# Performance work log

Measured on AMD Instinct MI355X. Metric: run time of the kernel, lower is better.

The kernel has to match this reference:

```python
import jax, jax.numpy as jnp
import numpy as np

L_IMG, L_TXT, B, C, T, D = 12, 12, 64, 1000, 8, 512


def setup_inputs() -> dict:
    key = jax.random.key(0)
    ks = jax.random.split(key, 8)
    s = 0.05  # keep attention logits in a sane range
    return {
        "x": jax.random.normal(ks[0], (L_IMG, B, D), jnp.float32),                 # per-layer projected CLS feats [L,B,D]
        "text_features": jax.random.normal(ks[1], (C, L_TXT, T, D), jnp.float32),  # precomputed per-class text feats
        "self_in_w": jax.random.normal(ks[2], (3 * D, D), jnp.float32) * s,
        "self_in_b": jnp.zeros((3 * D,), jnp.float32),
        "self_out_w": jax.random.normal(ks[3], (D, D), jnp.float32) * s,
        "self_out_b": jnp.zeros((D,), jnp.float32),
        "cross_in_w": jax.random.normal(ks[4], (3 * D, D), jnp.float32) * s,
        "cross_in_b": jnp.zeros((3 * D,), jnp.float32),
        "cross_out_w": jax.random.normal(ks[5], (D, D), jnp.float32) * s,
        "cross_out_b": jnp.zeros((D,), jnp.float32),
        "logit_scale": jnp.full((1,), np.log(1.0 / 0.07), jnp.float32),
    }


def reference(x, text_features, self_in_w, self_in_b, self_out_w, self_out_b,
              cross_in_w, cross_in_b, cross_out_w, cross_out_b, logit_scale):
    d = x.shape[-1]
    scale = 1.0 / jnp.sqrt(jnp.asarray(d, x.dtype))

    # ---- self-attention over the layer axis (torch MHA, 1 head, seq-first [L,B,D]) ----
    Wq, Wk, Wv = jnp.split(self_in_w, 3, axis=0)
    bq, bk, bv = jnp.split(self_in_b, 3, axis=0)
    q = jnp.einsum('lbd,ed->lbe', x, Wq) + bq
    k = jnp.einsum('lbd,ed->lbe', x, Wk) + bk
    v = jnp.einsum('lbd,ed->lbe', x, Wv) + bv
    attn = jax.nn.softmax(jnp.einsum('lbe,mbe->blm', q, k) * scale, axis=-1)
    xs = jnp.einsum('blm,mbe->lbe', attn, v) @ self_out_w.T + self_out_b   # [L,B,D]
    image_features = xs[-1]                                               # [B,D]

    # ---- batched cross-attention: query = image layer-tokens, key/value = per-class,
    #      per-template text layer-tokens; averaged over templates and query layers ----
    cWq, cWk, cWv = jnp.split(cross_in_w, 3, axis=0)
    cbq, cbk, cbv = jnp.split(cross_in_b, 3, axis=0)
    q2 = jnp.einsum('lbd,ed->lbe', xs, cWq) + cbq                          # [L,B,E]
    k2 = jnp.einsum('cmtd,ed->cmte', text_features, cWk) + cbk             # [C,M,T,E]
    v2 = jnp.einsum('cmtd,ed->cmte', text_features, cWv) + cbv
    a2 = jax.nn.softmax(jnp.einsum('lbe,cmte->bctlm', q2, k2) * scale, axis=-1)
    n_avg = a2.shape[2] * a2.shape[3]                                      # T * L_img
    # out_proj is linear, so mean over (template, layer) commutes with it
    ctx = jnp.einsum('bctlm,cmtd->bcd', a2, v2) / n_avg                    # [B,C,D]
    txt = ctx @ cross_out_w.T + cross_out_b                                # [B,C,D]

    # ---- normalize and compute logits (matching the source's permute(1,2,0) + norm(dim=-1)) ----
    tf = jnp.transpose(txt, (0, 2, 1))                                     # [B,D,C]
    img_n = image_features / jnp.linalg.norm(image_features, axis=-1, keepdims=True)
    tf_n = tf / jnp.linalg.norm(tf, axis=-1, keepdims=True)
    return jnp.exp(logit_scale[0]) * jnp.einsum('bd,bdc->bc', img_n, tf_n)  # [B,C]
```

## Files before the change

kernel.cpp:

```cpp
#include <hip/hip_runtime.h>

#define L_IMG 12
#define BATCH 64
#define NCLS  1000
#define DIM   512
#define NTM   96
#define SCALEF 0.044194173824159216f

typedef __attribute__((ext_vector_type(8))) short bf16x8;
typedef __attribute__((ext_vector_type(4))) float f32x4;

__device__ __forceinline__ float bf2f(unsigned short u) {
    return __uint_as_float(((unsigned int)u) << 16);
}
__device__ __forceinline__ unsigned short f2bf(float f) {
    unsigned int u = __float_as_uint(f);
    u += 0x7FFFu + ((u >> 16) & 1u);
    return (unsigned short)(u >> 16);
}
__device__ __forceinline__ void storeo(float* p, float v) { *p = v; }
__device__ __forceinline__ void storeo(unsigned short* p, float v) { *p = f2bf(v); }

__device__ __forceinline__ int swz(int row, int u) {
    return (row << 5) + ((u ^ ((row >> 1) & 3)) << 3);
}

__device__ __forceinline__ void gload16(const unsigned short* g, unsigned short* l) {
    __builtin_amdgcn_global_load_lds(
        (const __attribute__((address_space(1))) void*)g,
        (__attribute__((address_space(3))) void*)l, 16, 0, 0);
}

__global__ __launch_bounds__(256)
void f2bf_kernel(const float* __restrict__ in, unsigned short* __restrict__ out, int n)
{
    int i = (blockIdx.x * 256 + threadIdx.x) * 4;
    if (i < n) {
        float4 v = *(const float4*)(in + i);
        ushort4 o;
        o.x = f2bf(v.x); o.y = f2bf(v.y); o.z = f2bf(v.z); o.w = f2bf(v.w);
        *(ushort4*)(out + i) = o;
    }
}

__global__ __launch_bounds__(256)
void fold_wvo(const float* __restrict__ cow, const float* __restrict__ cWv,
              const float* __restrict__ cbv, const float* __restrict__ cob,
              unsigned short* __restrict__ Wvob, float* __restrict__ bvo)
{
    __shared__ float crow[DIM];
    __shared__ float red[256];
    const int d = blockIdx.x, t = threadIdx.x;
    float c0 = cow[d * DIM + t], c1 = cow[d * DIM + t + 256];
    crow[t] = c0; crow[t + 256] = c1;
    red[t] = c0 * cbv[t] + c1 * cbv[t + 256];
    __syncthreads();
    for (int s = 128; s > 0; s >>= 1) {
        if (t < s) red[t] += red[t + s];
        __syncthreads();
    }
    if (t == 0) bvo[d] = red[0] + cob[d];
    float a0 = 0.f, a1 = 0.f;
    for (int e = 0; e < DIM; e++) {
        float ce = crow[e];
        a0 += ce * cWv[e * DIM + t];
        a1 += ce * cWv[e * DIM + t + 256];
    }
    Wvob[d * DIM + t]       = f2bf(a0);
    Wvob[d * DIM + t + 256] = f2bf(a1);
}

#define BKT 32
#define LDT 68
__global__ __launch_bounds__(256)
void gemm_bt_f32(const float* __restrict__ A, const float* __restrict__ W,
                 const float* __restrict__ bias, float* __restrict__ Co,
                 int M, int N, int K, float out_scale)
{
    __shared__ float As[BKT * LDT];
    __shared__ float Ws[BKT * LDT];
    const int tid = threadIdx.x;
    const int m0 = blockIdx.y << 6, n0 = blockIdx.x << 6;
    const int tx = tid & 15, ty = tid >> 4;
    float acc[4][4] = {};
    for (int k0 = 0; k0 < K; k0 += BKT) {
        #pragma unroll
        for (int i = 0; i < 2; i++) {
            int slot = tid + (i << 8);
            int r = slot >> 3, kq = slot & 7;
            float4 v = *(const float4*)(A + (size_t)(m0 + r) * K + k0 + (kq << 2));
            As[(kq*4+0)*LDT + r] = v.x; As[(kq*4+1)*LDT + r] = v.y;
            As[(kq*4+2)*LDT + r] = v.z; As[(kq*4+3)*LDT + r] = v.w;
            float4 w = *(const float4*)(W + (size_t)(n0 + r) * K + k0 + (kq << 2));
            Ws[(kq*4+0)*LDT + r] = w.x; Ws[(kq*4+1)*LDT + r] = w.y;
            Ws[(kq*4+2)*LDT + r] = w.z; Ws[(kq*4+3)*LDT + r] = w.w;
        }
        __syncthreads();
        #pragma unroll
        for (int kk = 0; kk < BKT; kk++) {
            float4 a = *(const float4*)(As + kk*LDT + ty*4);
            float4 w = *(const float4*)(Ws + kk*LDT + tx*4);
            acc[0][0] += a.x*w.x; acc[0][1] += a.x*w.y; acc[0][2] += a.x*w.z; acc[0][3] += a.x*w.w;
            acc[1][0] += a.y*w.x; acc[1][1] += a.y*w.y; acc[1][2] += a.y*w.z; acc[1][3] += a.y*w.w;
            acc[2][0] += a.z*w.x; acc[2][1] += a.z*w.y; acc[2][2] += a.z*w.z; acc[2][3] += a.z*w.w;
            acc[3][0] += a.w*w.x; acc[3][1] += a.w*w.y; acc[3][2] += a.w*w.z; acc[3][3] += a.w*w.w;
        }
        __syncthreads();
    }
    #pragma unroll
    for (int i = 0; i < 4; i++) {
        int mr = m0 + ty*4 + i;
        #pragma unroll
        for (int j = 0; j < 4; j++) {
            int n = n0 + tx*4 + j;
            float v = acc[i][j];
            if (bias) v += bias[n];
            Co[(size_t)mr * N + n] = v * out_scale;
        }
    }
}

__global__ __launch_bounds__(256)
void gemm_nt_f32(const float* __restrict__ A, const float* __restrict__ W,
                 float* __restrict__ Co, int M, int N, int K)
{
    __shared__ float As[BKT * LDT];
    __shared__ float Ws[BKT * LDT];
    const int tid = threadIdx.x;
    const int m0 = blockIdx.y << 6, n0 = blockIdx.x << 6;
    const int tx = tid & 15, ty = tid >> 4;
    float acc[4][4] = {};
    for (int k0 = 0; k0 < K; k0 += BKT) {
        #pragma unroll
        for (int i = 0; i < 2; i++) {
            int slot = tid + (i << 8);
            int r = slot >> 3, kq = slot & 7;
            float4 v = *(const float4*)(A + (size_t)(m0 + r) * K + k0 + (kq << 2));
            As[(kq*4+0)*LDT + r] = v.x; As[(kq*4+1)*LDT + r] = v.y;
            As[(kq*4+2)*LDT + r] = v.z; As[(kq*4+3)*LDT + r] = v.w;
            int kr = slot >> 4, c4 = slot & 15;
            *(float4*)(Ws + kr*LDT + c4*4) =
                *(const float4*)(W + (size_t)(k0 + kr) * N + n0 + (c4 << 2));
        }
        __syncthreads();
        #pragma unroll
        for (int kk = 0; kk < BKT; kk++) {
            float4 a = *(const float4*)(As + kk*LDT + ty*4);
            float4 w = *(const float4*)(Ws + kk*LDT + tx*4);
            acc[0][0] += a.x*w.x; acc[0][1] += a.x*w.y; acc[0][2] += a.x*w.z; acc[0][3] += a.x*w.w;
            acc[1][0] += a.y*w.x; acc[1][1] += a.y*w.y; acc[1][2] += a.y*w.z; acc[1][3] += a.y*w.w;
            acc[2][0] += a.z*w.x; acc[2][1] += a.z*w.y; acc[2][2] += a.z*w.z; acc[2][3] += a.z*w.w;
            acc[3][0] += a.w*w.x; acc[3][1] += a.w*w.y; acc[3][2] += a.w*w.z; acc[3][3] += a.w*w.w;
        }
        __syncthreads();
    }
    #pragma unroll
    for (int i = 0; i < 4; i++) {
        int mr = m0 + ty*4 + i;
        #pragma unroll
        for (int j = 0; j < 4; j++)
            Co[(size_t)mr * N + n0 + tx*4 + j] = acc[i][j];
    }
}

__global__ __launch_bounds__(256)
void attn_kernel(const float* __restrict__ qkv, float* __restrict__ ao)
{
    __shared__ float lq[L_IMG * DIM];
    __shared__ float lk[L_IMG * DIM];
    __shared__ float sc[L_IMG * L_IMG];
    __shared__ float sa[L_IMG * L_IMG];
    const int b = blockIdx.x, tid = threadIdx.x;
    for (int i = 0; i < 6; i++) {
        int slot = tid + (i << 8);
        int l = slot >> 7, e4 = slot & 127;
        const float* row = qkv + (size_t)(l * BATCH + b) * 1536;
        *(float4*)(lq + l*DIM + e4*4) = *(const float4*)(row + e4*4);
        *(float4*)(lk + l*DIM + e4*4) = *(const float4*)(row + DIM + e4*4);
    }
    __syncthreads();
    if (tid < 144) {
        int l = tid / 12, m = tid % 12;
        float a = 0.f;
        for (int d4 = 0; d4 < 128; d4++) {
            float4 q = *(const float4*)(lq + l*DIM + d4*4);
            float4 k = *(const float4*)(lk + m*DIM + d4*4);
            a += q.x*k.x + q.y*k.y + q.z*k.z + q.w*k.w;
        }
        sc[tid] = a * SCALEF;
    }
    __syncthreads();
    if (tid < 12) {
        float mx = -1e30f;
        for (int m = 0; m < 12; m++) mx = fmaxf(mx, sc[tid*12 + m]);
        float e[12], s = 0.f;
        for (int m = 0; m < 12; m++) { e[m] = __expf(sc[tid*12 + m] - mx); s += e[m]; }
        float inv = 1.f / s;
        for (int m = 0; m < 12; m++) sa[tid*12 + m] = e[m] * inv;
    }
    __syncthreads();
    for (int i = 0; i < 2; i++) {
        int e = tid + (i << 8);
        float vv[12];
        #pragma unroll
        for (int m = 0; m < 12; m++)
            vv[m] = qkv[(size_t)(m * BATCH + b) * 1536 + 1024 + e];
        #pragma unroll
        for (int l = 0; l < 12; l++) {
            float a = 0.f;
            #pragma unroll
            for (int m = 0; m < 12; m++) a += sa[l*12 + m] * vv[m];
            ao[(size_t)(l * BATCH + b) * DIM + e] = a;
        }
    }
}

__global__ __launch_bounds__(256)
void img_kernel(const float* __restrict__ xs, float* __restrict__ imgn)
{
    __shared__ float red[256];
    const int b = blockIdx.x, tid = threadIdx.x;
    const float* row = xs + (size_t)(11 * BATCH + b) * DIM;
    float v0 = row[tid], v1 = row[tid + 256];
    red[tid] = v0*v0 + v1*v1;
    __syncthreads();
    for (int s = 128; s > 0; s >>= 1) {
        if (tid < s) red[tid] += red[tid + s];
        __syncthreads();
    }
    float inv = rsqrtf(red[0]);
    imgn[b*DIM + tid]       = v0 * inv;
    imgn[b*DIM + tid + 256] = v1 * inv;
}

__global__ __launch_bounds__(256)
void build_q2p(const float* __restrict__ q2s, unsigned short* __restrict__ q2pb)
{
    const int l = blockIdx.x, b = blockIdx.y, t = threadIdx.x;
    int d0 = t * 2;
    unsigned int o = 0;
    if (l < 12) {
        float2 v = *(const float2*)(q2s + (size_t)(l * BATCH + b) * DIM + d0);
        o = (unsigned int)f2bf(v.x) | ((unsigned int)f2bf(v.y) << 16);
    }
    ((unsigned int*)q2pb)[(size_t)(b * 16 + l) * 256 + t] = o;
}

template<typename OutT>
__global__ __launch_bounds__(256, 4)
void gemm_mfma(const unsigned short* __restrict__ A, const unsigned short* __restrict__ W,
               const float* __restrict__ bias, OutT* __restrict__ Co,
               int M, int N, float scale)
{
    const int K = DIM;
    __shared__ __align__(16) unsigned short AsBuf[2][128 * 32];
    __shared__ __align__(16) unsigned short WsBuf[2][128 * 32];
    const int m0 = blockIdx.y << 7, n0 = blockIdx.x << 7;
    const int tid = threadIdx.x;
    const int w = tid >> 6, lane = tid & 63;
    const int mt0 = (w & 1) * 4, nt0 = (w >> 1) * 4;
    const int r16 = lane & 15, kq = lane >> 4;
    const int row0 = (w << 5) + (lane >> 2), row1 = row0 + 16;
    const int sc0 = ((lane & 3) ^ ((row0 >> 1) & 3)) << 3;
    const int sc1 = ((lane & 3) ^ ((row1 >> 1) & 3)) << 3;
    const unsigned short* gA0 = A + (size_t)(m0 + row0) * K + sc0;
    const unsigned short* gA1 = A + (size_t)(m0 + row1) * K + sc1;
    const unsigned short* gW0 = W + (size_t)(n0 + row0) * K + sc0;
    const unsigned short* gW1 = W + (size_t)(n0 + row1) * K + sc1;
    const int lw = w << 10;
    int offa[4], offb[4];
    #pragma unroll
    for (int i = 0; i < 4; i++) {
        offa[i] = swz((mt0 + i) * 16 + r16, kq);
        offb[i] = swz((nt0 + i) * 16 + r16, kq);
    }
    f32x4 acc[4][4] = {};

    gload16(gA0, AsBuf[0] + lw);
    gload16(gA1, AsBuf[0] + lw + 512);
    gload16(gW0, WsBuf[0] + lw);
    gload16(gW1, WsBuf[0] + lw + 512);
    __syncthreads();

    #pragma unroll
    for (int t = 0; t < 16; t++) {
        const int cur = t & 1, nxt = cur ^ 1;
        if (t < 15) {
            const int ko = (t + 1) << 5;
            gload16(gA0 + ko, AsBuf[nxt] + lw);
            gload16(gA1 + ko, AsBuf[nxt] + lw + 512);
            gload16(gW0 + ko, WsBuf[nxt] + lw);
            gload16(gW1 + ko, WsBuf[nxt] + lw + 512);
        }
        bf16x8 af[4], bfr[4];
        #pragma unroll
        for (int i = 0; i < 4; i++) {
            af[i]  = *(const bf16x8*)(AsBuf[cur] + offa[i]);
            bfr[i] = *(const bf16x8*)(WsBuf[cur] + offb[i]);
        }
        #pragma unroll
        for (int i = 0; i < 4; i++)
            #pragma unroll
            for (int j = 0; j < 4; j++)
                acc[i][j] = __builtin_amdgcn_mfma_f32_16x16x32_bf16(af[i], bfr[j], acc[i][j], 0, 0, 0);
        if (t < 15) __syncthreads();
    }
    const int rbase = (lane >> 4) * 4;
    #pragma unroll
    for (int i = 0; i < 4; i++)
        #pragma unroll
        for (int j = 0; j < 4; j++) {
            int gcol = n0 + (nt0 + j) * 16 + r16;
            float bv = bias ? bias[gcol] : 0.f;
            #pragma unroll
            for (int r = 0; r < 4; r++) {
                int grow = m0 + (mt0 + i) * 16 + rbase + r;
                storeo(Co + (size_t)grow * N + gcol, acc[i][j][r] * scale + bv);
            }
        }
}

__global__ __launch_bounds__(256, 3)
void fused_scores(const unsigned short* __restrict__ q2pb, const unsigned short* __restrict__ k2,
                  float* __restrict__ wout)
{
    __shared__ __align__(16) unsigned short AsBuf[2][256 * 32];
    __shared__ __align__(16) unsigned short KsBuf[2][96 * 32];
    const int bid = blockIdx.x;
    const int g = bid >> 5, r = bid & 31;
    const int c = g * 8 + (r & 7), bg = r >> 3;
    const int tid = threadIdx.x;
    const int m0 = bg << 8;
    const int w = tid >> 6, lane = tid & 63;
    const int r16 = lane & 15, kq = lane >> 4;
    const size_t kb = (size_t)c * NTM * DIM;
    const int arow = lane >> 2, aun = lane & 3;
    const unsigned short* gAs[4];
    #pragma unroll
    for (int s = 0; s < 4; s++) {
        int rw = (w << 6) + (s << 4) + arow;
        int scx = (aun ^ ((rw >> 1) & 3)) << 3;
        gAs[s] = q2pb + (size_t)(m0 + rw) * DIM + scx;
    }
    const int krow0 = (w << 5) + arow, krow1 = krow0 + 16;
    const int sk0 = (aun ^ ((krow0 >> 1) & 3)) << 3;
    const int sk1 = (aun ^ ((krow1 >> 1) & 3)) << 3;
    const unsigned short* gK0 = k2 + kb + (size_t)krow0 * DIM + sk0;
    const unsigned short* gK1 = k2 + kb + (size_t)krow1 * DIM + sk1;
    const bool kw = (w < 3);
    const int lwA = w << 11;
    const int lwK = w << 10;
    int offa[4], offk[6];
    #pragma unroll
    for (int i = 0; i < 4; i++) offa[i] = swz((w << 6) + i * 16 + r16, kq);
    #pragma unroll
    for (int j = 0; j < 6; j++) offk[j] = swz(j * 16 + r16, kq);
    f32x4 acc[4][6] = {};

    #pragma unroll
    for (int s = 0; s < 4; s++) gload16(gAs[s], AsBuf[0] + lwA + (s << 9));
    if (kw) {
        gload16(gK0, KsBuf[0] + lwK);
        gload16(gK1, KsBuf[0] + lwK + 512);
    }
    __syncthreads();

    #pragma unroll
    for (int t = 0; t < 16; t++) {
        const int cur = t & 1, nxt = cur ^ 1;
        if (t < 15) {
            const int ko = (t + 1) << 5;
            #pragma unroll
            for (int s = 0; s < 4; s++) gload16(gAs[s] + ko, AsBuf[nxt] + lwA + (s << 9));
            if (kw) {
                gload16(gK0 + ko, KsBuf[nxt] + lwK);
                gload16(gK1 + ko, KsBuf[nxt] + lwK + 512);
            }
        }
        bf16x8 af[4], bfr[6];
        #pragma unroll
        for (int i = 0; i < 4; i++)
            af[i] = *(const bf16x8*)(AsBuf[cur] + offa[i]);
        #pragma unroll
        for (int j = 0; j < 6; j++)
            bfr[j] = *(const bf16x8*)(KsBuf[cur] + offk[j]);
        __builtin_amdgcn_s_setprio(1);
        #pragma unroll
        for (int i = 0; i < 4; i++)
            #pragma unroll
            for (int j = 0; j < 6; j++)
                acc[i][j] = __builtin_amdgcn_mfma_f32_16x16x32_bf16(af[i], bfr[j], acc[i][j], 0, 0, 0);
        __builtin_amdgcn_s_setprio(0);
        if (t < 15) __syncthreads();
    }

    #pragma unroll
    for (int i = 0; i < 4; i++) {
        #pragma unroll
        for (int rr = 0; rr < 4; rr++) {
            float v0 = acc[i][0][rr], v1 = acc[i][1][rr], v2 = acc[i][2][rr];
            float v3 = acc[i][3][rr], v4 = acc[i][4][rr], v5 = acc[i][5][rr];
            float mx = fmaxf(fmaxf(fmaxf(v0, v1), fmaxf(v2, v3)), fmaxf(v4, v5));
            mx = fmaxf(mx, __shfl_xor(mx, 8, 64));
            float e0 = __expf(v0 - mx), e1 = __expf(v1 - mx), e2 = __expf(v2 - mx);
            float e3 = __expf(v3 - mx), e4 = __expf(v4 - mx), e5 = __expf(v5 - mx);
            float s = e0 + e1 + e2 + e3 + e4 + e5;
            s += __shfl_xor(s, 8, 64);
            float inv = 1.f / (96.f * s);
            acc[i][0][rr] = e0 * inv; acc[i][1][rr] = e1 * inv; acc[i][2][rr] = e2 * inv;
            acc[i][3][rr] = e3 * inv; acc[i][4][rr] = e4 * inv; acc[i][5][rr] = e5 * inv;
        }
    }

    const bool contrib = (lane >> 4) < 3;
    #pragma unroll
    for (int i = 0; i < 4; i++) {
        float s6[6];
        #pragma unroll
        for (int j = 0; j < 6; j++) {
            float t = contrib ? (acc[i][j][0] + acc[i][j][1] + acc[i][j][2] + acc[i][j][3]) : 0.f;
            t += __shfl_xor(t, 16, 64);
            t += __shfl_xor(t, 32, 64);
            s6[j] = t;
        }
        if (lane < 16) {
            const int b = bg * 16 + (w << 2) + i;
            float* dst = wout + ((size_t)(b * NCLS + c)) * NTM;
            #pragma unroll
            for (int j = 0; j < 6; j++)
                dst[j * 16 + r16] = s6[j];
        }
    }
}

__global__ __launch_bounds__(256)
void ctx_kernel(const float* __restrict__ wbuf, const unsigned short* __restrict__ tfeb,
                unsigned short* __restrict__ ctxraw)
{
    __shared__ float ws[NTM * 16];
    const int bid = blockIdx.x;
    const int g = bid >> 5, r = bid & 31;
    const int c = g * 8 + (r & 7), bg = r >> 3;
    const int tid = threadIdx.x;
    for (int idx = tid; idx < 16 * NTM; idx += 256) {
        int bl = idx / NTM, tm = idx - bl * NTM;
        ws[tm * 16 + bl] = wbuf[((size_t)((bg * 16 + bl) * NCLS + c)) * NTM + tm];
    }
    __syncthreads();
    float a0[16] = {}, a1[16] = {};
    const unsigned int* vrow = (const unsigned int*)(tfeb + (size_t)c * NTM * DIM) + tid;
    #pragma unroll 4
    for (int tm = 0; tm < NTM; tm++) {
        unsigned int u = vrow[tm * 256];
        float vx = __uint_as_float(u << 16);
        float vy = __uint_as_float(u & 0xFFFF0000u);
        float wq[16];
        *(float4*)(wq + 0)  = *(const float4*)(ws + tm * 16 + 0);
        *(float4*)(wq + 4)  = *(const float4*)(ws + tm * 16 + 4);
        *(float4*)(wq + 8)  = *(const float4*)(ws + tm * 16 + 8);
        *(float4*)(wq + 12) = *(const float4*)(ws + tm * 16 + 12);
        #pragma unroll
        for (int bl = 0; bl < 16; bl++) {
            a0[bl] += wq[bl] * vx; a1[bl] += wq[bl] * vy;
        }
    }
    #pragma unroll
    for (int bl = 0; bl < 16; bl++) {
        int b = bg * 16 + bl;
        unsigned int o = (unsigned int)f2bf(a0[bl]) | ((unsigned int)f2bf(a1[bl]) << 16);
        ((unsigned int*)ctxraw)[(size_t)(b * NCLS + c) * 256 + tid] = o;
    }
}

__global__ __launch_bounds__(256)
void n2_kernel(const unsigned short* __restrict__ txt, float* __restrict__ n2)
{
    const int b = blockIdx.x, cg = blockIdx.y, t = threadIdx.x;
    float a0 = 0.f, a1 = 0.f;
    const unsigned int* p = (const unsigned int*)txt + ((size_t)(b * NCLS + cg * 125)) * 256 + t;
    for (int c = 0; c < 125; c++) {
        unsigned int u = p[c * 256];
        float vx = __uint_as_float(u << 16);
        float vy = __uint_as_float(u & 0xFFFF0000u);
        a0 += vx * vx; a1 += vy * vy;
    }
    atomicAdd(&n2[b * DIM + t * 2], a0);
    atomicAdd(&n2[b * DIM + t * 2 + 1], a1);
}

__global__ __launch_bounds__(256)
void logits_kernel(const unsigned short* __restrict__ txt, const float* __restrict__ imgn,
                   const float* __restrict__ n2, const float* __restrict__ logit_scale,
                   float* __restrict__ out)
{
    __shared__ float lu[DIM];
    const int b = blockIdx.y, cg = blockIdx.x, tid = threadIdx.x;
    float els = expf(logit_scale[0]);
    lu[tid]       = els * imgn[b*DIM + tid]       * rsqrtf(n2[b*DIM + tid]);
    lu[tid + 256] = els * imgn[b*DIM + tid + 256] * rsqrtf(n2[b*DIM + tid + 256]);
    __syncthreads();
    int wave = tid >> 6, lane = tid & 63;
    int c = (cg << 2) + wave;
    const unsigned short* row = txt + (size_t)(b * NCLS + c) * DIM;
    ushort4 p0 = ((const ushort4*)row)[lane*2];
    ushort4 p1 = ((const ushort4*)row)[lane*2 + 1];
    int d0 = lane * 8;
    float s = bf2f(p0.x)*lu[d0]   + bf2f(p0.y)*lu[d0+1] + bf2f(p0.z)*lu[d0+2] + bf2f(p0.w)*lu[d0+3]
            + bf2f(p1.x)*lu[d0+4] + bf2f(p1.y)*lu[d0+5] + bf2f(p1.z)*lu[d0+6] + bf2f(p1.w)*lu[d0+7];
    #pragma unroll
    for (int off = 32; off > 0; off >>= 1) s += __shfl_down(s, off, 64);
    if (lane == 0) out[b*NCLS + c] = s;
}

extern "C" void kernel_launch(void* const* d_in, const int* in_sizes, int n_in,
                              void* d_out, int out_size, void* d_ws, size_t ws_size,
                              hipStream_t stream)
{
    const float* x   = (const float*)d_in[0];
    const float* tfe = (const float*)d_in[1];
    const float* siw = (const float*)d_in[2];
    const float* sib = (const float*)d_in[3];
    const float* sow = (const float*)d_in[4];
    const float* sob = (const float*)d_in[5];
    const float* ciw = (const float*)d_in[6];
    const float* cib = (const float*)d_in[7];
    const float* cow = (const float*)d_in[8];
    const float* cob = (const float*)d_in[9];
    const float* ls  = (const float*)d_in[10];
    float* out = (float*)d_out;

    char* p = (char*)d_ws;
    auto alloc = [&](size_t bytes) { char* r = p; p += (bytes + 255) & ~255ull; return r; };
    unsigned short* tfeb   = (unsigned short*)alloc((size_t)49152000 * 2);
    unsigned short* ctxraw = (unsigned short*)alloc((size_t)BATCH * NCLS * DIM * 2);
    float* wbuf            = (float*)alloc((size_t)BATCH * NCLS * NTM * 4);
    float* qkv             = (float*)alloc((size_t)768 * 1536 * 4);
    float* ao              = (float*)alloc((size_t)768 * DIM * 4);
    float* xs              = (float*)alloc((size_t)768 * DIM * 4);
    float* q2s             = (float*)alloc((size_t)768 * DIM * 4);
    float* q2k             = (float*)alloc((size_t)768 * DIM * 4);
    unsigned short* q2pb   = (unsigned short*)alloc((size_t)1024 * DIM * 2);
    unsigned short* Wvob   = (unsigned short*)alloc((size_t)DIM * DIM * 2);
    float* bvo             = (float*)alloc(DIM * 4);
    float* n2              = (float*)alloc(BATCH * DIM * 4);
    float* imgn            = (float*)alloc(BATCH * DIM * 4);
    unsigned short* txt    = tfeb;

    hipMemsetAsync(n2, 0, BATCH * DIM * 4, stream);

    f2bf_kernel<<<48000, 256, 0, stream>>>(tfe, tfeb, 49152000);
    fold_wvo<<<512, 256, 0, stream>>>(cow, ciw + 1024*512, cib + 1024, cob, Wvob, bvo);

    gemm_bt_f32<<<dim3(24, 12), 256, 0, stream>>>(x, siw, sib, qkv, 768, 1536, 512, 1.f);
    attn_kernel<<<64, 256, 0, stream>>>(qkv, ao);
    gemm_bt_f32<<<dim3(8, 12), 256, 0, stream>>>(ao, sow, sob, xs, 768, 512, 512, 1.f);
    img_kernel<<<64, 256, 0, stream>>>(xs, imgn);
    gemm_bt_f32<<<dim3(8, 12), 256, 0, stream>>>(xs, ciw, cib, q2s, 768, 512, 512, SCALEF);
    gemm_nt_f32<<<dim3(8, 12), 256, 0, stream>>>(q2s, ciw + 512*512, q2k, 768, 512, 512);
    build_q2p<<<dim3(16, 64), 256, 0, stream>>>(q2k, q2pb);

    fused_scores<<<4000, 256, 0, stream>>>(q2pb, tfeb, wbuf);

    ctx_kernel<<<4000, 256, 0, stream>>>(wbuf, tfeb, ctxraw);

    gemm_mfma<unsigned short><<<dim3(4, 500), 256, 0, stream>>>(
        ctxraw, Wvob, bvo, txt, 64000, 512, 1.f);

    n2_kernel<<<dim3(64, 8), 256, 0, stream>>>(txt, n2);
    logits_kernel<<<dim3(250, 64), 256, 0, stream>>>(txt, imgn, n2, ls, out);
}
```

Baseline: 762.7 us.

## Drop zero-padded query rows in scores kernel and fuse column norms into GEMM epilogue

The packed query buffer no longer pads each batch's 12 layer rows to 16, so the scores kernel tiles 192 real rows per block instead of 256. That removes wasted MFMA work and A-tile loads, and the smaller shared-memory footprint allows a higher occupancy hint. Per-batch reduction of the layer rows now goes through LDS atomics. Separately, the squared column norms are accumulated in the output-projection GEMM epilogue with wave shuffles and global atomics, which removes the separate n2 pass over the text features. In exchange there is extra epilogue and atomic work, and the fused norms are computed from fp32 values rather than the rounded bf16 outputs.

```diff
diff --git a/kernel.cpp b/kernel.cpp
--- a/kernel.cpp
+++ b/kernel.cpp
@@ -234,23 +234,20 @@
 }
 
 __global__ __launch_bounds__(256)
-void build_q2p(const float* __restrict__ q2s, unsigned short* __restrict__ q2pb)
+void build_q2p(const float* __restrict__ q2s, unsigned short* __restrict__ q2pk)
 {
     const int l = blockIdx.x, b = blockIdx.y, t = threadIdx.x;
     int d0 = t * 2;
-    unsigned int o = 0;
-    if (l < 12) {
-        float2 v = *(const float2*)(q2s + (size_t)(l * BATCH + b) * DIM + d0);
-        o = (unsigned int)f2bf(v.x) | ((unsigned int)f2bf(v.y) << 16);
-    }
-    ((unsigned int*)q2pb)[(size_t)(b * 16 + l) * 256 + t] = o;
+    float2 v = *(const float2*)(q2s + (size_t)(l * BATCH + b) * DIM + d0);
+    unsigned int o = (unsigned int)f2bf(v.x) | ((unsigned int)f2bf(v.y) << 16);
+    ((unsigned int*)q2pk)[(size_t)(b * 12 + l) * 256 + t] = o;
 }
 
 template<typename OutT>
 __global__ __launch_bounds__(256, 4)
 void gemm_mfma(const unsigned short* __restrict__ A, const unsigned short* __restrict__ W,
                const float* __restrict__ bias, OutT* __restrict__ Co,
-               int M, int N, float scale)
+               int M, int N, float scale, float* __restrict__ n2)
 {
     const int K = DIM;
     __shared__ __align__(16) unsigned short AsBuf[2][128 * 32];
@@ -306,41 +303,54 @@
         if (t < 15) __syncthreads();
     }
     const int rbase = (lane >> 4) * 4;
-    #pragma unroll
-    for (int i = 0; i < 4; i++)
-        #pragma unroll
-        for (int j = 0; j < 4; j++) {
-            int gcol = n0 + (nt0 + j) * 16 + r16;
-            float bv = bias ? bias[gcol] : 0.f;
+    const int b0 = m0 / NCLS;
+    const int splitrow = (b0 + 1) * NCLS;
+    #pragma unroll
+    for (int j = 0; j < 4; j++) {
+        int gcol = n0 + (nt0 + j) * 16 + r16;
+        float bv = bias ? bias[gcol] : 0.f;
+        float s0 = 0.f, s1 = 0.f;
+        #pragma unroll
+        for (int i = 0; i < 4; i++)
             #pragma unroll
             for (int r = 0; r < 4; r++) {
                 int grow = m0 + (mt0 + i) * 16 + rbase + r;
-                storeo(Co + (size_t)grow * N + gcol, acc[i][j][r] * scale + bv);
+                float v = acc[i][j][r] * scale + bv;
+                storeo(Co + (size_t)grow * N + gcol, v);
+                if (n2) { if (grow < splitrow) s0 += v * v; else s1 += v * v; }
             }
-        }
-}
-
-__global__ __launch_bounds__(256, 3)
-void fused_scores(const unsigned short* __restrict__ q2pb, const unsigned short* __restrict__ k2,
+        if (n2) {
+            s0 += __shfl_xor(s0, 16, 64); s0 += __shfl_xor(s0, 32, 64);
+            s1 += __shfl_xor(s1, 16, 64); s1 += __shfl_xor(s1, 32, 64);
+            if (lane < 16) {
+                atomicAdd(&n2[(size_t)b0 * N + gcol], s0);
+                if (splitrow < m0 + 128) atomicAdd(&n2[(size_t)(b0 + 1) * N + gcol], s1);
+            }
+        }
+    }
+}
+
+__global__ __launch_bounds__(256, 4)
+void fused_scores(const unsigned short* __restrict__ q2pk, const unsigned short* __restrict__ k2,
                   float* __restrict__ wout)
 {
-    __shared__ __align__(16) unsigned short AsBuf[2][256 * 32];
+    __shared__ __align__(16) unsigned short AsBuf[2][192 * 32];
     __shared__ __align__(16) unsigned short KsBuf[2][96 * 32];
     const int bid = blockIdx.x;
-    const int g = bid >> 5, r = bid & 31;
-    const int c = g * 8 + (r & 7), bg = r >> 3;
+    const int g8 = bid >> 5, r = bid & 31;
+    const int c = g8 * 8 + (r & 7), bg = r >> 3;
     const int tid = threadIdx.x;
-    const int m0 = bg << 8;
+    const int m0 = bg * 192;
     const int w = tid >> 6, lane = tid & 63;
     const int r16 = lane & 15, kq = lane >> 4;
     const size_t kb = (size_t)c * NTM * DIM;
     const int arow = lane >> 2, aun = lane & 3;
-    const unsigned short* gAs[4];
-    #pragma unroll
-    for (int s = 0; s < 4; s++) {
-        int rw = (w << 6) + (s << 4) + arow;
+    const unsigned short* gAs[3];
+    #pragma unroll
+    for (int s = 0; s < 3; s++) {
+        int rw = w * 48 + (s << 4) + arow;
         int scx = (aun ^ ((rw >> 1) & 3)) << 3;
-        gAs[s] = q2pb + (size_t)(m0 + rw) * DIM + scx;
+        gAs[s] = q2pk + (size_t)(m0 + rw) * DIM + scx;
     }
     const int krow0 = (w << 5) + arow, krow1 = krow0 + 16;
     const int sk0 = (aun ^ ((krow0 >> 1) & 3)) << 3;
@@ -348,17 +358,17 @@
     const unsigned short* gK0 = k2 + kb + (size_t)krow0 * DIM + sk0;
     const unsigned short* gK1 = k2 + kb + (size_t)krow1 * DIM + sk1;
     const bool kw = (w < 3);
-    const int lwA = w << 11;
+    const int lwA = w * 1536;
     const int lwK = w << 10;
-    int offa[4], offk[6];
-    #pragma unroll
-    for (int i = 0; i < 4; i++) offa[i] = swz((w << 6) + i * 16 + r16, kq);
+    int offa[3], offk[6];
+    #pragma unroll
+    for (int i = 0; i < 3; i++) offa[i] = swz(w * 48 + i * 16 + r16, kq);
     #pragma unroll
     for (int j = 0; j < 6; j++) offk[j] = swz(j * 16 + r16, kq);
-    f32x4 acc[4][6] = {};
-
-    #pragma unroll
-    for (int s = 0; s < 4; s++) gload16(gAs[s], AsBuf[0] + lwA + (s << 9));
+    f32x4 acc[3][6] = {};
+
+    #pragma unroll
+    for (int s = 0; s < 3; s++) gload16(gAs[s], AsBuf[0] + lwA + (s << 9));
     if (kw) {
         gload16(gK0, KsBuf[0] + lwK);
         gload16(gK1, KsBuf[0] + lwK + 512);
@@ -371,22 +381,22 @@
         if (t < 15) {
             const int ko = (t + 1) << 5;
             #pragma unroll
-            for (int s = 0; s < 4; s++) gload16(gAs[s] + ko, AsBuf[nxt] + lwA + (s << 9));
+            for (int s = 0; s < 3; s++) gload16(gAs[s] + ko, AsBuf[nxt] + lwA + (s << 9));
             if (kw) {
                 gload16(gK0 + ko, KsBuf[nxt] + lwK);
                 gload16(gK1 + ko, KsBuf[nxt] + lwK + 512);
             }
         }
-        bf16x8 af[4], bfr[6];
-        #pragma unroll
-        for (int i = 0; i < 4; i++)
+        bf16x8 af[3], bfr[6];
+        #pragma unroll
+        for (int i = 0; i < 3; i++)
             af[i] = *(const bf16x8*)(AsBuf[cur] + offa[i]);
         #pragma unroll
         for (int j = 0; j < 6; j++)
             bfr[j] = *(const bf16x8*)(KsBuf[cur] + offk[j]);
         __builtin_amdgcn_s_setprio(1);
         #pragma unroll
-        for (int i = 0; i < 4; i++)
+        for (int i = 0; i < 3; i++)
             #pragma unroll
             for (int j = 0; j < 6; j++)
                 acc[i][j] = __builtin_amdgcn_mfma_f32_16x16x32_bf16(af[i], bfr[j], acc[i][j], 0, 0, 0);
@@ -395,7 +405,7 @@
     }
 
     #pragma unroll
-    for (int i = 0; i < 4; i++) {
+    for (int i = 0; i < 3; i++) {
         #pragma unroll
         for (int rr = 0; rr < 4; rr++) {
             float v0 = acc[i][0][rr], v1 = acc[i][1][rr], v2 = acc[i][2][rr];
@@ -412,24 +422,28 @@
         }
     }
 
-    const bool contrib = (lane >> 4) < 3;
-    #pragma unroll
-    for (int i = 0; i < 4; i++) {
-        float s6[6];
+    float* red = (float*)AsBuf[0];
+    float* myred = red + w * 384;
+    #pragma unroll
+    for (int k = 0; k < 6; k++) myred[k * 64 + lane] = 0.f;
+    __syncthreads();
+    const int g = lane >> 4;
+    #pragma unroll
+    for (int i = 0; i < 3; i++) {
+        int bl = (4 * i + g) / 3;
         #pragma unroll
         for (int j = 0; j < 6; j++) {
-            float t = contrib ? (acc[i][j][0] + acc[i][j][1] + acc[i][j][2] + acc[i][j][3]) : 0.f;
-            t += __shfl_xor(t, 16, 64);
-            t += __shfl_xor(t, 32, 64);
-            s6[j] = t;
-        }
-        if (lane < 16) {
-            const int b = bg * 16 + (w << 2) + i;
-            float* dst = wout + ((size_t)(b * NCLS + c)) * NTM;
-            #pragma unroll
-            for (int j = 0; j < 6; j++)
-                dst[j * 16 + r16] = s6[j];
-        }
+            float t = acc[i][j][0] + acc[i][j][1] + acc[i][j][2] + acc[i][j][3];
+            atomicAdd(&myred[bl * 96 + j * 16 + r16], t);
+        }
+    }
+    __syncthreads();
+    const int bbase = bg * 16 + (w << 2);
+    #pragma unroll
+    for (int k = 0; k < 6; k++) {
+        int idx = k * 64 + lane;
+        int bl = idx / 96, col = idx - bl * 96;
+        wout[((size_t)((bbase + bl) * NCLS + c)) * NTM + col] = myred[idx];
     }
 }
 
@@ -473,22 +487,6 @@
 }
 
 __global__ __launch_bounds__(256)
-void n2_kernel(const unsigned short* __restrict__ txt, float* __restrict__ n2)
-{
-    const int b = blockIdx.x, cg = blockIdx.y, t = threadIdx.x;
-    float a0 = 0.f, a1 = 0.f;
-    const unsigned int* p = (const unsigned int*)txt + ((size_t)(b * NCLS + cg * 125)) * 256 + t;
-    for (int c = 0; c < 125; c++) {
-        unsigned int u = p[c * 256];
-        float vx = __uint_as_float(u << 16);
-        float vy = __uint_as_float(u & 0xFFFF0000u);
-        a0 += vx * vx; a1 += vy * vy;
-    }
-    atomicAdd(&n2[b * DIM + t * 2], a0);
-    atomicAdd(&n2[b * DIM + t * 2 + 1], a1);
-}
-
-__global__ __launch_bounds__(256)
 void logits_kernel(const unsigned short* __restrict__ txt, const float* __restrict__ imgn,
                    const float* __restrict__ n2, const float* __restrict__ logit_scale,
                    float* __restrict__ out)
@@ -539,7 +537,7 @@
     float* xs              = (float*)alloc((size_t)768 * DIM * 4);
     float* q2s             = (float*)alloc((size_t)768 * DIM * 4);
     float* q2k             = (float*)alloc((size_t)768 * DIM * 4);
-    unsigned short* q2pb   = (unsigned short*)alloc((size_t)1024 * DIM * 2);
+    unsigned short* q2pk   = (unsigned short*)alloc((size_t)768 * DIM * 2);
     unsigned short* Wvob   = (unsigned short*)alloc((size_t)DIM * DIM * 2);
     float* bvo             = (float*)alloc(DIM * 4);
     float* n2              = (float*)alloc(BATCH * DIM * 4);
@@ -557,15 +555,14 @@
     img_kernel<<<64, 256, 0, stream>>>(xs, imgn);
     gemm_bt_f32<<<dim3(8, 12), 256, 0, stream>>>(xs, ciw, cib, q2s, 768, 512, 512, SCALEF);
     gemm_nt_f32<<<dim3(8, 12), 256, 0, stream>>>(q2s, ciw + 512*512, q2k, 768, 512, 512);
-    build_q2p<<<dim3(16, 64), 256, 0, stream>>>(q2k, q2pb);
-
-    fused_scores<<<4000, 256, 0, stream>>>(q2pb, tfeb, wbuf);
+    build_q2p<<<dim3(12, 64), 256, 0, stream>>>(q2k, q2pk);
+
+    fused_scores<<<4000, 256, 0, stream>>>(q2pk, tfeb, wbuf);
 
     ctx_kernel<<<4000, 256, 0, stream>>>(wbuf, tfeb, ctxraw);
 
     gemm_mfma<unsigned short><<<dim3(4, 500), 256, 0, stream>>>(
-        ctxraw, Wvob, bvo, txt, 64000, 512, 1.f);
-
-    n2_kernel<<<dim3(64, 8), 256, 0, stream>>>(txt, n2);
+        ctxraw, Wvob, bvo, txt, 64000, 512, 1.f, n2);
+
     logits_kernel<<<dim3(250, 64), 256, 0, stream>>>(txt, imgn, n2, ls, out);
 }
```

New measurement: 810.7 us. +6.3%, slower.
